# Performance work log

Measured on AMD Instinct MI355X. Metric: run time of the kernel, lower is better.

## Reference

```python
import jax, jax.numpy as jnp
import numpy as np

N_NODES = 100000

def _gcn_conv(x, W, b, src, dst, n_nodes):
    # PyG GCNConv: h = x @ W; add self-loops; deg over dst; norm = d^-1/2[src]*d^-1/2[dst];
    # out = scatter_add(norm * h[src] -> dst) + b
    h = x @ W  # [N, out]
    deg = jax.ops.segment_sum(jnp.ones_like(dst, dtype=x.dtype), dst, num_segments=n_nodes)
    dinv = jnp.where(deg > 0, jax.lax.rsqrt(deg), 0.0)
    norm = dinv[src] * dinv[dst]  # [E]
    msg = h[src] * norm[:, None]  # [E, out]
    out = jax.ops.segment_sum(msg, dst, num_segments=n_nodes)
    return out + b

def setup_inputs() -> dict:
    key = jax.random.key(0)
    k1, k2, k3, k4 = jax.random.split(key, 4)
    x = jax.random.normal(k1, (N_NODES, 165), dtype=jnp.float32)
    edge_index = jax.random.randint(k2, (2, 1600000), 0, N_NODES, dtype=jnp.int64)
    # glorot-ish init for weights
    W1 = jax.random.normal(k3, (165, 128), dtype=jnp.float32) * (1.0 / np.sqrt(165))
    b1 = jnp.zeros((128,), dtype=jnp.float32)
    W4 = jax.random.normal(k4, (128, 1), dtype=jnp.float32) * (1.0 / np.sqrt(128))
    b4 = jnp.zeros((1,), dtype=jnp.float32)
    return {"x": x, "edge_index": edge_index, "W1": W1, "b1": b1, "W4": W4, "b4": b4}

def reference(x, edge_index, W1, b1, W4, b4):
    n = x.shape[0]
    loop = jnp.arange(n, dtype=edge_index.dtype)
    src = jnp.concatenate([edge_index[0], loop])  # add self-loops
    dst = jnp.concatenate([edge_index[1], loop])
    h = _gcn_conv(x, W1, b1, src, dst, n)
    h = jax.nn.relu(h)
    # dropout p=0.1 is identity at inference (training=False)
    out = _gcn_conv(h, W4, b4, src, dst, n)
    return jax.nn.sigmoid(out)
```

## Files before the change

### kernel.cpp

```cpp
#include <hip/hip_runtime.h>
#include <math.h>

#define N_NODES 100000

using bf16x8 = __attribute__((ext_vector_type(8))) short;
using f32x4  = __attribute__((ext_vector_type(4))) float;

static inline size_t align_up(size_t x, size_t a){ return (x + a - 1) & ~(a - 1); }

__device__ __forceinline__ unsigned short f2bf(float f){
  unsigned u = __float_as_uint(f);
  u = (u + 0x7fffu + ((u >> 16) & 1u)) >> 16;
  return (unsigned short)u;
}
__device__ __forceinline__ float bf2f(unsigned short h){
  return __uint_as_float(((unsigned)h) << 16);
}
__device__ __forceinline__ float bf_lo(unsigned u){ return __uint_as_float(u << 16); }
__device__ __forceinline__ float bf_hi(unsigned u){ return __uint_as_float(u & 0xffff0000u); }

__device__ __forceinline__ int xcd_id(){
  int x;
  asm volatile("s_getreg_b32 %0, hwreg(HW_REG_XCC_ID)" : "=s"(x));
  return x & 7;
}

__global__ void k_zero(int* __restrict__ p, int n){
  int i = blockIdx.x*blockDim.x + threadIdx.x;
  if(i < n) p[i] = 0;
}

__global__ void k_convert_count(const int* __restrict__ ei,
                                int* __restrict__ rank, int* __restrict__ cnt8,
                                int E, int n){
  __shared__ int s_is64;
  if(threadIdx.x == 0){
    int is64 = 1;
    for(int k=0;k<64;k++){ if(ei[2*k+1] != 0){ is64 = 0; break; } }
    s_is64 = is64;
  }
  __syncthreads();
  int is64 = s_is64;
  int r = xcd_id();
  int* my = cnt8 + (size_t)r * n;
  int stride = gridDim.x * blockDim.x;
  for(int e = blockIdx.x*blockDim.x + threadIdx.x; e < E; e += stride){
    int d = is64 ? ei[2*(E + e)] : ei[E + e];
    int local = atomicAdd(&my[d], 1);
    rank[e] = (local << 3) | r;
  }
}

__global__ void k_scan_part(const int* __restrict__ cnt8, int* __restrict__ bsum, int n){
  __shared__ int red[256];
  int b = blockIdx.x, t = threadIdx.x;
  int base = b*1024 + t*4;
  int s = 0;
  #pragma unroll
  for(int k=0;k<4;k++){
    int i = base + k;
    if(i < n){
      #pragma unroll
      for(int r=0;r<8;r++) s += cnt8[(size_t)r*n + i];
    }
  }
  red[t] = s; __syncthreads();
  for(int off=128; off>0; off>>=1){
    if(t < off) red[t] += red[t+off];
    __syncthreads();
  }
  if(t==0) bsum[b] = red[0];
}

__global__ void k_scan_top(int* __restrict__ bsum, int nb){
  __shared__ int sh[128];
  int t = threadIdx.x;
  int v = (t < nb) ? bsum[t] : 0;
  sh[t] = v; __syncthreads();
  int inc = v;
  for(int off=1; off<128; off<<=1){
    int add = (t >= off) ? sh[t-off] : 0;
    __syncthreads();
    inc += add; sh[t] = inc;
    __syncthreads();
  }
  if(t < nb) bsum[t] = inc - v;
}

__global__ void k_scan_down(int* __restrict__ cnt8, const int* __restrict__ bsum,
                            int* __restrict__ offs, float* __restrict__ dinv, int n, int E){
  __shared__ int sh[256];
  int b = blockIdx.x, t = threadIdx.x;
  int base = b*1024 + t*4;
  int tot[4]; int local = 0;
  #pragma unroll
  for(int k=0;k<4;k++){
    int i = base + k; int s = 0;
    if(i < n){
      #pragma unroll
      for(int r=0;r<8;r++) s += cnt8[(size_t)r*n + i];
    }
    tot[k] = s; local += s;
  }
  sh[t] = local; __syncthreads();
  int inc = local;
  for(int off=1; off<256; off<<=1){
    int add = (t >= off) ? sh[t-off] : 0;
    __syncthreads();
    inc += add; sh[t] = inc;
    __syncthreads();
  }
  int running = bsum[b] + (inc - local);
  #pragma unroll
  for(int k=0;k<4;k++){
    int i = base + k;
    if(i < n){
      offs[i] = running;
      dinv[i] = rsqrtf((float)(tot[k] + 1));
      int acc = running;
      #pragma unroll
      for(int r=0;r<8;r++){
        int c = cnt8[(size_t)r*n + i];
        cnt8[(size_t)r*n + i] = acc;
        acc += c;
      }
      running += tot[k];
    }
  }
  if(b==0 && t==0) offs[n] = E;
}

__global__ void k_fill(const int* __restrict__ ei, const int* __restrict__ rank,
                       const int* __restrict__ cbase, int* __restrict__ csr, int E, int n){
  __shared__ int s_is64;
  if(threadIdx.x == 0){
    int is64 = 1;
    for(int k=0;k<64;k++){ if(ei[2*k+1] != 0){ is64 = 0; break; } }
    s_is64 = is64;
  }
  __syncthreads();
  int is64 = s_is64;
  int stride = gridDim.x * blockDim.x;
  for(int e = blockIdx.x*blockDim.x + threadIdx.x; e < E; e += stride){
    int s, d;
    if(is64){ s = ei[2*e]; d = ei[2*(E + e)]; }
    else    { s = ei[e];   d = ei[E + e]; }
    int rk = rank[e];
    csr[cbase[(size_t)(rk & 7)*n + d] + (rk >> 3)] = s;
  }
}

__global__ void k_prep_w1(const float* __restrict__ w1, unsigned short* __restrict__ w1b){
  int id = blockIdx.x*blockDim.x + threadIdx.x;
  if(id >= 6*8*64) return;
  int lane = id & 63;
  int st = id >> 6;
  int s = st >> 3, t = st & 7;
  int g = lane >> 4;
  int nn = t*16 + (lane & 15);
  unsigned short* dst = w1b + (size_t)((s*8 + t)*64 + lane)*16;
  #pragma unroll
  for(int j=0;j<8;j++){
    int k = s*32 + g*8 + j;
    float v = (k < 165) ? w1[(size_t)k*128 + nn] : 0.f;
    unsigned short hi = f2bf(v);
    unsigned short lo = f2bf(v - bf2f(hi));
    dst[j] = hi; dst[8+j] = lo;
  }
}

__global__ __launch_bounds__(256) void k_gemm_mfma(const float* __restrict__ x,
                                                   const unsigned short* __restrict__ w1b,
                                                   const float* __restrict__ dinv,
                                                   unsigned short* __restrict__ hsc, int n){
  __shared__ float xs[64*172];
  int t = threadIdx.x;
  int rowbase = blockIdx.x*64;
  int nrow = min(64, n - rowbase);
  int nfl = nrow * 165;
  const float* xblk = x + (size_t)rowbase*165;
  for(int f = t; f < nfl; f += 256){
    int r = f / 165;
    int c = f - r*165;
    xs[r*172 + c] = xblk[f];
  }
  __syncthreads();

  int lane = threadIdx.x & 63;
  int w    = threadIdx.x >> 6;
  int m    = lane & 15;
  int g    = lane >> 4;
  int row  = rowbase + w*16 + m;
  const float* xr = xs + (w*16 + m)*172;
  const bf16x8* wb = (const bf16x8*)w1b;

  f32x4 acc[8];
  #pragma unroll
  for(int q=0;q<8;q++){ acc[q][0]=0.f; acc[q][1]=0.f; acc[q][2]=0.f; acc[q][3]=0.f; }

  #pragma unroll
  for(int s=0;s<6;s++){
    int k0 = s*32 + g*8;
    float v[8];
    if(s < 5){
      #pragma unroll
      for(int j=0;j<8;j++) v[j] = xr[k0+j];
    }else{
      #pragma unroll
      for(int j=0;j<8;j++){ int k = k0+j; v[j] = (k < 165) ? xr[k] : 0.f; }
    }
    bf16x8 ah, al;
    #pragma unroll
    for(int j=0;j<8;j++){
      unsigned short hi = f2bf(v[j]);
      ah[j] = (short)hi;
      al[j] = (short)f2bf(v[j] - bf2f(hi));
    }
    #pragma unroll
    for(int q=0;q<8;q++){
      int bidx = ((s*8 + q)*64 + lane)*2;
      bf16x8 bh = wb[bidx];
      bf16x8 bl = wb[bidx + 1];
      acc[q] = __builtin_amdgcn_mfma_f32_16x16x32_bf16(bh, ah, acc[q], 0, 0, 0);
      acc[q] = __builtin_amdgcn_mfma_f32_16x16x32_bf16(bh, al, acc[q], 0, 0, 0);
      acc[q] = __builtin_amdgcn_mfma_f32_16x16x32_bf16(bl, ah, acc[q], 0, 0, 0);
    }
  }

  if(row < n){
    float di = dinv[row];
    unsigned* hp = (unsigned*)(hsc + (size_t)row*128);
    #pragma unroll
    for(int q=0;q<8;q++){
      unsigned short q0 = f2bf(acc[q][0]*di);
      unsigned short q1 = f2bf(acc[q][1]*di);
      unsigned short q2 = f2bf(acc[q][2]*di);
      unsigned short q3 = f2bf(acc[q][3]*di);
      int nbase = q*16 + g*4;
      hp[(nbase>>1)    ] = (unsigned)q0 | ((unsigned)q1 << 16);
      hp[(nbase>>1) + 1] = (unsigned)q2 | ((unsigned)q3 << 16);
    }
  }
}

__global__ __launch_bounds__(256) void k_agg1(const unsigned short* __restrict__ hsc,
                                              const int* __restrict__ offs,
                                              const int* __restrict__ csr,
                                              const float* __restrict__ dinv,
                                              const float* __restrict__ b1,
                                              const float* __restrict__ w4,
                                              float* __restrict__ g, int n){
  int wv = threadIdx.x >> 6;
  int lane = threadIdx.x & 63;
  int q   = lane >> 4;
  int sub = lane & 15;
  int i = blockIdx.x * 4 + wv;
  if(i >= n) return;

  float di = dinv[i];
  int s0 = offs[i], s1 = offs[i+1];
  const uint4* base = (const uint4*)hsc;

  float a0=0.f,a1=0.f,a2=0.f,a3=0.f,a4=0.f,a5=0.f,a6=0.f,a7=0.f;
  int e = s0 + q;
  for(; e + 4 < s1; e += 8){
    uint4 uA = base[(size_t)csr[e]*16 + sub];
    uint4 uB = base[(size_t)csr[e+4]*16 + sub];
    a0 += bf_lo(uA.x) + bf_lo(uB.x);  a1 += bf_hi(uA.x) + bf_hi(uB.x);
    a2 += bf_lo(uA.y) + bf_lo(uB.y);  a3 += bf_hi(uA.y) + bf_hi(uB.y);
    a4 += bf_lo(uA.z) + bf_lo(uB.z);  a5 += bf_hi(uA.z) + bf_hi(uB.z);
    a6 += bf_lo(uA.w) + bf_lo(uB.w);  a7 += bf_hi(uA.w) + bf_hi(uB.w);
  }
  if(e < s1){
    uint4 uA = base[(size_t)csr[e]*16 + sub];
    a0 += bf_lo(uA.x);  a1 += bf_hi(uA.x);
    a2 += bf_lo(uA.y);  a3 += bf_hi(uA.y);
    a4 += bf_lo(uA.z);  a5 += bf_hi(uA.z);
    a6 += bf_lo(uA.w);  a7 += bf_hi(uA.w);
  }
  if(q == 0){
    uint4 uS = base[(size_t)i*16 + sub];
    a0 += bf_lo(uS.x);  a1 += bf_hi(uS.x);
    a2 += bf_lo(uS.y);  a3 += bf_hi(uS.y);
    a4 += bf_lo(uS.z);  a5 += bf_hi(uS.z);
    a6 += bf_lo(uS.w);  a7 += bf_hi(uS.w);
  }
  a0 += __shfl_xor(a0,16,64); a0 += __shfl_xor(a0,32,64);
  a1 += __shfl_xor(a1,16,64); a1 += __shfl_xor(a1,32,64);
  a2 += __shfl_xor(a2,16,64); a2 += __shfl_xor(a2,32,64);
  a3 += __shfl_xor(a3,16,64); a3 += __shfl_xor(a3,32,64);
  a4 += __shfl_xor(a4,16,64); a4 += __shfl_xor(a4,32,64);
  a5 += __shfl_xor(a5,16,64); a5 += __shfl_xor(a5,32,64);
  a6 += __shfl_xor(a6,16,64); a6 += __shfl_xor(a6,32,64);
  a7 += __shfl_xor(a7,16,64); a7 += __shfl_xor(a7,32,64);

  int f = sub*8;
  float4 bL = *(const float4*)&b1[f];
  float4 bH = *(const float4*)&b1[f+4];
  float4 wL = *(const float4*)&w4[f];
  float4 wH = *(const float4*)&w4[f+4];
  float p = fmaxf(di*a0 + bL.x, 0.f)*wL.x
          + fmaxf(di*a1 + bL.y, 0.f)*wL.y
          + fmaxf(di*a2 + bL.z, 0.f)*wL.z
          + fmaxf(di*a3 + bL.w, 0.f)*wL.w
          + fmaxf(di*a4 + bH.x, 0.f)*wH.x
          + fmaxf(di*a5 + bH.y, 0.f)*wH.y
          + fmaxf(di*a6 + bH.z, 0.f)*wH.z
          + fmaxf(di*a7 + bH.w, 0.f)*wH.w;
  p += __shfl_xor(p, 1, 64);
  p += __shfl_xor(p, 2, 64);
  p += __shfl_xor(p, 4, 64);
  p += __shfl_xor(p, 8, 64);
  if(lane == 0) g[i] = di * p;
}

__global__ void k_agg2c(const float* __restrict__ g, const int* __restrict__ offs,
                        const int* __restrict__ csr, const float* __restrict__ dinv,
                        const float* __restrict__ b4, float* __restrict__ out, int n){
  int lane = threadIdx.x & 63;
  int wv   = threadIdx.x >> 6;
  int sub  = lane & 7;
  int i = blockIdx.x*32 + wv*8 + (lane >> 3);
  if(i >= n) return;
  int s1 = offs[i+1];
  float p = 0.f;
  for(int e = offs[i] + sub; e < s1; e += 8) p += g[csr[e]];
  p += __shfl_xor(p, 4, 8);
  p += __shfl_xor(p, 2, 8);
  p += __shfl_xor(p, 1, 8);
  if(sub == 0){
    float di = dinv[i];
    float z = di*(p + g[i]) + b4[0];
    out[i] = 1.f/(1.f+expf(-z));
  }
}

extern "C" void kernel_launch(void* const* d_in, const int* in_sizes, int n_in,
                              void* d_out, int out_size, void* d_ws, size_t ws_size,
                              hipStream_t stream){
  const float* x  = (const float*)d_in[0];
  const int*   ei = (const int*)d_in[1];
  const float* w1 = (const float*)d_in[2];
  const float* b1 = (const float*)d_in[3];
  const float* w4 = (const float*)d_in[4];
  const float* b4 = (const float*)d_in[5];
  float* out = (float*)d_out;

  const int n = N_NODES;
  const int E = in_sizes[1] / 2;

  char* ws = (char*)d_ws;
  size_t off = 0;
  auto carve = [&](size_t bytes)->void*{
    void* p = ws + off; off = align_up(off + bytes, 256); return p;
  };
  int*   cnt8 = (int*)carve((size_t)8*n*4);
  int*   offs = (int*)carve((size_t)(n+1)*4);
  int*   bsum = (int*)carve(128*4);
  float* dinv = (float*)carve((size_t)n*4);
  int*   rank = (int*)carve((size_t)E*4);
  int*   csr  = (int*)carve((size_t)E*4);
  unsigned short* w1b = (unsigned short*)carve((size_t)6*8*64*16*2);
  unsigned short* hsc = (unsigned short*)carve((size_t)n*128*2);
  float* g    = (float*)carve((size_t)n*4);
  (void)ws_size;

  int nb = (n + 1023) / 1024;

  k_zero         <<<(8*n+255)/256, 256, 0, stream>>>(cnt8, 8*n);
  k_convert_count<<<2048, 256, 0, stream>>>(ei, rank, cnt8, E, n);
  k_scan_part    <<<nb, 256, 0, stream>>>(cnt8, bsum, n);
  k_scan_top     <<<1, 128, 0, stream>>>(bsum, nb);
  k_scan_down    <<<nb, 256, 0, stream>>>(cnt8, bsum, offs, dinv, n, E);
  k_fill         <<<2048, 256, 0, stream>>>(ei, rank, cnt8, csr, E, n);
  k_prep_w1      <<<12, 256, 0, stream>>>(w1, w1b);
  k_gemm_mfma    <<<(n+63)/64, 256, 0, stream>>>(x, w1b, dinv, hsc, n);
  k_agg1         <<<(n+3)/4, 256, 0, stream>>>(hsc, offs, csr, dinv, b1, w4, g, n);
  k_agg2c        <<<(n+31)/32, 256, 0, stream>>>(g, offs, csr, dinv, b4, out, n);
}
```

Measured before the change: 323.1 us.

## Build CSR with second atomic pass instead of stored per-edge ranks; unroll gather

The CSR build no longer stores a per-edge rank array during counting. The fill pass now re-derives slot positions with atomics on the scanned per-bucket counters. Buckets are chosen by block index over contiguous edge chunks instead of by hardware XCD id, and the CSR writes use nontemporal stores. This removes the rank buffer's 4E-byte write and read but adds a second round of atomics, and neighbor order within a row becomes nondeterministic. The layer-1 aggregation also gains a 4-way unrolled gather loop to keep more loads in flight.

```diff
diff --git a/kernel.cpp b/kernel.cpp
--- a/kernel.cpp
+++ b/kernel.cpp
@@ -19,20 +19,13 @@
 __device__ __forceinline__ float bf_lo(unsigned u){ return __uint_as_float(u << 16); }
 __device__ __forceinline__ float bf_hi(unsigned u){ return __uint_as_float(u & 0xffff0000u); }
 
-__device__ __forceinline__ int xcd_id(){
-  int x;
-  asm volatile("s_getreg_b32 %0, hwreg(HW_REG_XCC_ID)" : "=s"(x));
-  return x & 7;
-}
-
 __global__ void k_zero(int* __restrict__ p, int n){
   int i = blockIdx.x*blockDim.x + threadIdx.x;
   if(i < n) p[i] = 0;
 }
 
-__global__ void k_convert_count(const int* __restrict__ ei,
-                                int* __restrict__ rank, int* __restrict__ cnt8,
-                                int E, int n){
+__global__ void k_count(const int* __restrict__ ei, int* __restrict__ cnt8,
+                        int E, int n, int epb){
   __shared__ int s_is64;
   if(threadIdx.x == 0){
     int is64 = 1;
@@ -41,13 +34,12 @@
   }
   __syncthreads();
   int is64 = s_is64;
-  int r = xcd_id();
-  int* my = cnt8 + (size_t)r * n;
-  int stride = gridDim.x * blockDim.x;
-  for(int e = blockIdx.x*blockDim.x + threadIdx.x; e < E; e += stride){
+  int* my = cnt8 + (size_t)(blockIdx.x & 7) * n;
+  int lo = blockIdx.x * epb;
+  int hi = min(lo + epb, E);
+  for(int e = lo + threadIdx.x; e < hi; e += 256){
     int d = is64 ? ei[2*(E + e)] : ei[E + e];
-    int local = atomicAdd(&my[d], 1);
-    rank[e] = (local << 3) | r;
+    atomicAdd(&my[d], 1);
   }
 }
 
@@ -130,8 +122,8 @@
   if(b==0 && t==0) offs[n] = E;
 }
 
-__global__ void k_fill(const int* __restrict__ ei, const int* __restrict__ rank,
-                       const int* __restrict__ cbase, int* __restrict__ csr, int E, int n){
+__global__ void k_fill(const int* __restrict__ ei, int* __restrict__ cbase,
+                       int* __restrict__ csr, int E, int n, int epb){
   __shared__ int s_is64;
   if(threadIdx.x == 0){
     int is64 = 1;
@@ -140,13 +132,15 @@
   }
   __syncthreads();
   int is64 = s_is64;
-  int stride = gridDim.x * blockDim.x;
-  for(int e = blockIdx.x*blockDim.x + threadIdx.x; e < E; e += stride){
+  int* my = cbase + (size_t)(blockIdx.x & 7) * n;
+  int lo = blockIdx.x * epb;
+  int hi = min(lo + epb, E);
+  for(int e = lo + threadIdx.x; e < hi; e += 256){
     int s, d;
     if(is64){ s = ei[2*e]; d = ei[2*(E + e)]; }
     else    { s = ei[e];   d = ei[E + e]; }
-    int rk = rank[e];
-    csr[cbase[(size_t)(rk & 7)*n + d] + (rk >> 3)] = s;
+    int pos = atomicAdd(&my[d], 1);
+    __builtin_nontemporal_store(s, &csr[pos]);
   }
 }
 
@@ -263,20 +257,35 @@
 
   float a0=0.f,a1=0.f,a2=0.f,a3=0.f,a4=0.f,a5=0.f,a6=0.f,a7=0.f;
   int e = s0 + q;
+  for(; e + 12 < s1; e += 16){
+    int i0=csr[e], i1=csr[e+4], i2=csr[e+8], i3=csr[e+12];
+    uint4 u0 = base[(size_t)i0*16 + sub];
+    uint4 u1 = base[(size_t)i1*16 + sub];
+    uint4 u2 = base[(size_t)i2*16 + sub];
+    uint4 u3 = base[(size_t)i3*16 + sub];
+    a0 += (bf_lo(u0.x)+bf_lo(u1.x)) + (bf_lo(u2.x)+bf_lo(u3.x));
+    a1 += (bf_hi(u0.x)+bf_hi(u1.x)) + (bf_hi(u2.x)+bf_hi(u3.x));
+    a2 += (bf_lo(u0.y)+bf_lo(u1.y)) + (bf_lo(u2.y)+bf_lo(u3.y));
+    a3 += (bf_hi(u0.y)+bf_hi(u1.y)) + (bf_hi(u2.y)+bf_hi(u3.y));
+    a4 += (bf_lo(u0.z)+bf_lo(u1.z)) + (bf_lo(u2.z)+bf_lo(u3.z));
+    a5 += (bf_hi(u0.z)+bf_hi(u1.z)) + (bf_hi(u2.z)+bf_hi(u3.z));
+    a6 += (bf_lo(u0.w)+bf_lo(u1.w)) + (bf_lo(u2.w)+bf_lo(u3.w));
+    a7 += (bf_hi(u0.w)+bf_hi(u1.w)) + (bf_hi(u2.w)+bf_hi(u3.w));
+  }
   for(; e + 4 < s1; e += 8){
-    uint4 uA = base[(size_t)csr[e]*16 + sub];
-    uint4 uB = base[(size_t)csr[e+4]*16 + sub];
-    a0 += bf_lo(uA.x) + bf_lo(uB.x);  a1 += bf_hi(uA.x) + bf_hi(uB.x);
-    a2 += bf_lo(uA.y) + bf_lo(uB.y);  a3 += bf_hi(uA.y) + bf_hi(uB.y);
-    a4 += bf_lo(uA.z) + bf_lo(uB.z);  a5 += bf_hi(uA.z) + bf_hi(uB.z);
-    a6 += bf_lo(uA.w) + bf_lo(uB.w);  a7 += bf_hi(uA.w) + bf_hi(uB.w);
+    uint4 u0 = base[(size_t)csr[e]*16 + sub];
+    uint4 u1 = base[(size_t)csr[e+4]*16 + sub];
+    a0 += bf_lo(u0.x)+bf_lo(u1.x);  a1 += bf_hi(u0.x)+bf_hi(u1.x);
+    a2 += bf_lo(u0.y)+bf_lo(u1.y);  a3 += bf_hi(u0.y)+bf_hi(u1.y);
+    a4 += bf_lo(u0.z)+bf_lo(u1.z);  a5 += bf_hi(u0.z)+bf_hi(u1.z);
+    a6 += bf_lo(u0.w)+bf_lo(u1.w);  a7 += bf_hi(u0.w)+bf_hi(u1.w);
   }
   if(e < s1){
-    uint4 uA = base[(size_t)csr[e]*16 + sub];
-    a0 += bf_lo(uA.x);  a1 += bf_hi(uA.x);
-    a2 += bf_lo(uA.y);  a3 += bf_hi(uA.y);
-    a4 += bf_lo(uA.z);  a5 += bf_hi(uA.z);
-    a6 += bf_lo(uA.w);  a7 += bf_hi(uA.w);
+    uint4 u0 = base[(size_t)csr[e]*16 + sub];
+    a0 += bf_lo(u0.x);  a1 += bf_hi(u0.x);
+    a2 += bf_lo(u0.y);  a3 += bf_hi(u0.y);
+    a4 += bf_lo(u0.z);  a5 += bf_hi(u0.z);
+    a6 += bf_lo(u0.w);  a7 += bf_hi(u0.w);
   }
   if(q == 0){
     uint4 uS = base[(size_t)i*16 + sub];
@@ -348,6 +357,7 @@
 
   const int n = N_NODES;
   const int E = in_sizes[1] / 2;
+  const int epb = (E + 2047) / 2048;
 
   char* ws = (char*)d_ws;
   size_t off = 0;
@@ -358,7 +368,6 @@
   int*   offs = (int*)carve((size_t)(n+1)*4);
   int*   bsum = (int*)carve(128*4);
   float* dinv = (float*)carve((size_t)n*4);
-  int*   rank = (int*)carve((size_t)E*4);
   int*   csr  = (int*)carve((size_t)E*4);
   unsigned short* w1b = (unsigned short*)carve((size_t)6*8*64*16*2);
   unsigned short* hsc = (unsigned short*)carve((size_t)n*128*2);
@@ -367,14 +376,14 @@
 
   int nb = (n + 1023) / 1024;
 
-  k_zero         <<<(8*n+255)/256, 256, 0, stream>>>(cnt8, 8*n);
-  k_convert_count<<<2048, 256, 0, stream>>>(ei, rank, cnt8, E, n);
-  k_scan_part    <<<nb, 256, 0, stream>>>(cnt8, bsum, n);
-  k_scan_top     <<<1, 128, 0, stream>>>(bsum, nb);
-  k_scan_down    <<<nb, 256, 0, stream>>>(cnt8, bsum, offs, dinv, n, E);
-  k_fill         <<<2048, 256, 0, stream>>>(ei, rank, cnt8, csr, E, n);
-  k_prep_w1      <<<12, 256, 0, stream>>>(w1, w1b);
-  k_gemm_mfma    <<<(n+63)/64, 256, 0, stream>>>(x, w1b, dinv, hsc, n);
-  k_agg1         <<<(n+3)/4, 256, 0, stream>>>(hsc, offs, csr, dinv, b1, w4, g, n);
-  k_agg2c        <<<(n+31)/32, 256, 0, stream>>>(g, offs, csr, dinv, b4, out, n);
-}
+  k_zero     <<<(8*n+255)/256, 256, 0, stream>>>(cnt8, 8*n);
+  k_count    <<<2048, 256, 0, stream>>>(ei, cnt8, E, n, epb);
+  k_scan_part<<<nb, 256, 0, stream>>>(cnt8, bsum, n);
+  k_scan_top <<<1, 128, 0, stream>>>(bsum, nb);
+  k_scan_down<<<nb, 256, 0, stream>>>(cnt8, bsum, offs, dinv, n, E);
+  k_fill     <<<2048, 256, 0, stream>>>(ei, cnt8, csr, E, n, epb);
+  k_prep_w1  <<<12, 256, 0, stream>>>(w1, w1b);
+  k_gemm_mfma<<<(n+63)/64, 256, 0, stream>>>(x, w1b, dinv, hsc, n);
+  k_agg1     <<<(n+3)/4, 256, 0, stream>>>(hsc, offs, csr, dinv, b1, w4, g, n);
+  k_agg2c    <<<(n+31)/32, 256, 0, stream>>>(g, offs, csr, dinv, b4, out, n);
+}
```

Measured after the change: 440.7 us. +36.4%, slower.
